# Optimization experiments

Hardware: AMD Instinct MI355X
Metric: run time of the kernel (lower is better)

The kernel has to match this reference:

```python
import jax, jax.numpy as jnp
import numpy as np

N, D, C, P = 256, 1024, 4, 46  # nodes, embedding_dim, max children, num dependency labels
NEG = -1e30  # masked-out candidate value for the max-reduce


def setup_inputs() -> dict:
    key = jax.random.key(0)
    k1, k2 = jax.random.split(key)
    embeddings = jax.random.normal(k1, (N, D), dtype=jnp.float32)
    # Xavier-uniform init of the per-dependency [D,D] matrices, as in _init_params
    scale = float(np.sqrt(6.0 / (D + D)))
    params = jax.random.uniform(k2, (P, D, D), dtype=jnp.float32, minval=-scale, maxval=scale)
    # Build a random tree in topological order: children of node i have index < i;
    # node N-1 is the root. Padded child slots are masked out.
    rng = np.random.default_rng(0)
    c_idx = np.zeros((N, C), dtype=np.int32)
    c_mask = np.zeros((N, C), dtype=bool)
    for i in range(1, N):
        n_children = int(rng.integers(0, C + 1))  # 0 => leaf-like internal node
        c_idx[i] = rng.integers(0, i, size=C)
        c_mask[i, :n_children] = True
    c_mask[N - 1, :] = True  # root always has children
    c_dep = rng.integers(0, P, size=(N, C)).astype(np.int32)
    return {
        "embeddings": embeddings,
        "params": params,
        "children_idx": jnp.asarray(c_idx),
        "children_dep": jnp.asarray(c_dep),
        "children_mask": jnp.asarray(c_mask),
    }


def reference(embeddings, params, children_idx, children_dep, children_mask):
    """Tree-structured dependency encoder.

    For each node i (children first, topological order):
      leaf:     z_i = x_i
      internal: cand_c = params[dep_c] * relu(z_child_c)[None, :]   # [D, D] per child
                mult   = max over children of cand_c                 # [D, D]
                z_i    = x_i @ mult                                  # [D]
    Returns the root embedding, shape [1, D] (matches torch output).
    """
    n_nodes, d = embeddings.shape

    def step(z, inp):
        i, c_idx, c_dep, c_mask = inp
        child_z = jax.nn.relu(z[c_idx])                      # [C, D]
        cand = params[c_dep] * child_z[:, None, :]           # [C, D, D]
        cand = jnp.where(c_mask[:, None, None], cand, NEG)
        mult = jnp.max(cand, axis=0)                         # [D, D]
        x = embeddings[i]                                    # [D]
        z_i = jnp.where(jnp.any(c_mask), x @ mult, x)
        return z.at[i].set(z_i), None

    z0 = jnp.zeros_like(embeddings)
    idxs = jnp.arange(n_nodes)
    z, _ = jax.lax.scan(step, z0, (idxs, children_idx, children_dep, children_mask))
    return z[-1:]  # root node is last in topological order -> [1, D]
```

## Files before the change

kernel.cpp:

```cpp
#include <hip/hip_runtime.h>
#include <hip/hip_fp16.h>
#include <cstddef>

#define NN 256
#define DD 1024
#define CC 4
#define NP 46
#define NT 512
#define ROOT (NN - 1)

__device__ __half g_Pth[NP][DD][DD];

__global__ __launch_bounds__(256) void transpose_kernel(
    const float* __restrict__ par) {
  __shared__ float tile[128][65];
  const int b = blockIdx.x;
  const int p = b >> 7;
  const int t = b & 127;
  const int tr = (t >> 4) << 7;
  const int tc = (t & 15) << 6;
  const int tid = threadIdx.x;
  const float* src = par + ((size_t)p << 20);
  __half* dst = &g_Pth[p][0][0];

#pragma unroll
  for (int k = 0; k < 8; ++k) {
    const int idx = tid + (k << 8);
    const int row = idx >> 4;
    const int c4 = (idx & 15) << 2;
    const float4 v = *(const float4*)(src + (size_t)(tr + row) * DD + tc + c4);
    tile[row][c4 + 0] = v.x;
    tile[row][c4 + 1] = v.y;
    tile[row][c4 + 2] = v.z;
    tile[row][c4 + 3] = v.w;
  }
  __syncthreads();

  const int l = tid & 63;
  const int cb = (tid >> 6) << 4;
  const int r4 = (l & 31) << 2;
#pragma unroll
  for (int m = 0; m < 8; ++m) {
    const int c = cb + (m << 1) + (l >> 5);
    const __half2 h01 = __floats2half2_rn(tile[r4 + 0][c], tile[r4 + 1][c]);
    const __half2 h23 = __floats2half2_rn(tile[r4 + 2][c], tile[r4 + 3][c]);
    const unsigned int u0 = *(const unsigned int*)&h01;
    const unsigned int u1 = *(const unsigned int*)&h23;
    const unsigned long long u =
        (unsigned long long)u0 | ((unsigned long long)u1 << 32);
    __builtin_nontemporal_store(
        u, (unsigned long long*)(dst + (size_t)(tc + c) * DD + tr + r4));
  }
}

struct St {
  float2 p0, p1, p2, p3;
  float x0, x1;
};

__device__ __forceinline__ float4 relu4(float4 v) {
  float4 r;
  r.x = fmaxf(v.x, 0.f); r.y = fmaxf(v.y, 0.f);
  r.z = fmaxf(v.z, 0.f); r.w = fmaxf(v.w, 0.f);
  return r;
}

__device__ __forceinline__ void ld_stage(St& S, int e,
                                         const __half* __restrict__ pt,
                                         const float* __restrict__ emb,
                                         const short* e_meta, const short* e_node,
                                         int j0, int r2) {
  const int meta = e_meta[e];
  const int dep = meta & 0x1FFF;
  const __half* hb = pt + (((size_t)dep) << 20) + (((size_t)j0) << 10) + r2;
  S.p0 = __half22float2(*(const __half2*)(hb));
  S.p1 = __half22float2(*(const __half2*)(hb + DD));
  S.p2 = __half22float2(*(const __half2*)(hb + 2 * DD));
  S.p3 = __half22float2(*(const __half2*)(hb + 3 * DD));
  if (meta & 0x8000) {
    const float2 xx = *(const float2*)(emb + (((size_t)e_node[e]) << 10) + r2);
    S.x0 = xx.x; S.x1 = xx.y;
  }
}

__device__ __forceinline__ float2 mul2s(float2 a, float s) {
  float2 r; r.x = a.x * s; r.y = a.y * s; return r;
}
__device__ __forceinline__ float2 max2(float2 a, float2 b) {
  float2 r; r.x = fmaxf(a.x, b.x); r.y = fmaxf(a.y, b.y); return r;
}

__device__ __forceinline__ void cmp_stage(const St& S, int e, float2& m0, float2& m1,
                                          float2& m2, float2& m3,
                                          float (*z_loc)[4], float (*s_part)[4],
                                          const short* e_child, const short* e_meta,
                                          const short* e_node, int tid) {
  const int meta = e_meta[e];
  const float4 u = relu4(*(const float4*)z_loc[e_child[e]]);
  if (meta & (1 << 14)) {
    m0 = mul2s(S.p0, u.x); m1 = mul2s(S.p1, u.y);
    m2 = mul2s(S.p2, u.z); m3 = mul2s(S.p3, u.w);
  } else {
    m0 = max2(m0, mul2s(S.p0, u.x)); m1 = max2(m1, mul2s(S.p1, u.y));
    m2 = max2(m2, mul2s(S.p2, u.z)); m3 = max2(m3, mul2s(S.p3, u.w));
  }
  if (meta & 0x8000) {
    float4 acc;
    acc.x = fmaf(S.x1, m0.y, S.x0 * m0.x);
    acc.y = fmaf(S.x1, m1.y, S.x0 * m1.x);
    acc.z = fmaf(S.x1, m2.y, S.x0 * m2.x);
    acc.w = fmaf(S.x1, m3.y, S.x0 * m3.x);
#pragma unroll
    for (int off = 1; off < 64; off <<= 1) {
      acc.x += __shfl_xor(acc.x, off, 64);
      acc.y += __shfl_xor(acc.y, off, 64);
      acc.z += __shfl_xor(acc.z, off, 64);
      acc.w += __shfl_xor(acc.w, off, 64);
    }
    if ((tid & 63) == 0) *(float4*)s_part[tid >> 6] = acc;
    __syncthreads();
    if (tid < 4) {
      float s = 0.f;
#pragma unroll
      for (int k = 0; k < 8; ++k) s += s_part[k][tid];
      z_loc[e_node[e]][tid] = s;
    }
    __syncthreads();
  }
}

__global__ __launch_bounds__(NT, 1) void walk_kernel(
    const float* __restrict__ emb, const int* __restrict__ cidx,
    const int* __restrict__ cdep, const unsigned char* __restrict__ cmask,
    float* __restrict__ out) {
  __shared__ float z_loc[NN][4];
  __shared__ short s_ci[NN][CC];
  __shared__ short s_cd[NN][CC];
  __shared__ short s_nc[NN];
  __shared__ int s_pfx[NN];
  __shared__ unsigned char s_reach[NN];
  __shared__ short s_e_child[NN * CC];
  __shared__ short s_e_meta[NN * CC];
  __shared__ short s_e_node[NN * CC];
  __shared__ int s_NE;
  __shared__ int s_flag;
  __shared__ float s_part[8][4];

  const int tid = threadIdx.x;
  const int j0 = blockIdx.x << 2;
  const int r2 = tid << 1;
  const __half* pt = &g_Pth[0][0][0];

  if (tid == 0)
    s_flag = (cmask[1021] == 1 && cmask[1022] == 1 && cmask[1023] == 1);
  __syncthreads();
  const bool m_u8 = (s_flag != 0);
  const int* m32 = (const int*)cmask;
  if (tid < NN) {
    int nc = 0;
#pragma unroll
    for (int c = 0; c < CC; ++c) {
      bool mk = m_u8 ? (cmask[tid * CC + c] != 0) : (m32[tid * CC + c] != 0);
      if (mk) {
        s_ci[tid][nc] = (short)cidx[tid * CC + c];
        s_cd[tid][nc] = (short)cdep[tid * CC + c];
        ++nc;
      }
    }
    s_nc[tid] = (short)nc;
    s_reach[tid] = (tid == ROOT) ? 1 : 0;
  }
  __syncthreads();

  for (int it = 0; it < NN + 2; ++it) {
    if (tid == 0) s_flag = 0;
    __syncthreads();
    if (tid < NN && s_reach[tid] && s_nc[tid] > 0) {
      for (int c = 0; c < s_nc[tid]; ++c) {
        const int ch = s_ci[tid][c];
        if (!s_reach[ch]) { s_reach[ch] = 1; s_flag = 1; }
      }
    }
    __syncthreads();
    const int chg = s_flag;
    __syncthreads();
    if (!chg) break;
  }

  const int wgt = (tid < NN && s_reach[tid] && s_nc[tid] > 0) ? (int)s_nc[tid] : 0;
  if (tid < NN) s_pfx[tid] = wgt;
  __syncthreads();
  for (int off = 1; off < NN; off <<= 1) {
    int v = 0;
    if (tid < NN && tid >= off) v = s_pfx[tid - off];
    __syncthreads();
    if (tid < NN) s_pfx[tid] += v;
    __syncthreads();
  }
  if (tid < NN && wgt > 0) {
    const int st = s_pfx[tid] - wgt;
    for (int c = 0; c < wgt; ++c) {
      s_e_child[st + c] = s_ci[tid][c];
      int meta = (int)s_cd[tid][c];
      if (c == 0) meta |= 1 << 14;
      if (c == wgt - 1) meta |= 1 << 15;
      s_e_meta[st + c] = (short)meta;
      s_e_node[st + c] = (short)tid;
    }
  }
  if (tid == NN - 1) s_NE = s_pfx[NN - 1];

  if (tid < NN) {
    const float4 e = *(const float4*)(emb + (((size_t)tid) << 10) + j0);
    *(float4*)z_loc[tid] = e;
  }
  __syncthreads();
  const int NE = s_NE;

  St A, B, C, D;
  float2 m0, m1, m2, m3;
  if (NE > 0) ld_stage(A, 0, pt, emb, s_e_meta, s_e_node, j0, r2);
  if (NE > 1) ld_stage(B, 1, pt, emb, s_e_meta, s_e_node, j0, r2);
  if (NE > 2) ld_stage(C, 2, pt, emb, s_e_meta, s_e_node, j0, r2);
  int e = 0;
  while (e < NE) {
    if (e + 3 < NE) ld_stage(D, e + 3, pt, emb, s_e_meta, s_e_node, j0, r2);
    cmp_stage(A, e, m0, m1, m2, m3, z_loc, s_part, s_e_child, s_e_meta, s_e_node, tid);
    if (++e >= NE) break;
    if (e + 3 < NE) ld_stage(A, e + 3, pt, emb, s_e_meta, s_e_node, j0, r2);
    cmp_stage(B, e, m0, m1, m2, m3, z_loc, s_part, s_e_child, s_e_meta, s_e_node, tid);
    if (++e >= NE) break;
    if (e + 3 < NE) ld_stage(B, e + 3, pt, emb, s_e_meta, s_e_node, j0, r2);
    cmp_stage(C, e, m0, m1, m2, m3, z_loc, s_part, s_e_child, s_e_meta, s_e_node, tid);
    if (++e >= NE) break;
    if (e + 3 < NE) ld_stage(C, e + 3, pt, emb, s_e_meta, s_e_node, j0, r2);
    cmp_stage(D, e, m0, m1, m2, m3, z_loc, s_part, s_e_child, s_e_meta, s_e_node, tid);
    ++e;
  }

  if (tid < 4) out[j0 + tid] = z_loc[ROOT][tid];
}

extern "C" void kernel_launch(void* const* d_in, const int* in_sizes, int n_in,
                              void* d_out, int out_size, void* d_ws, size_t ws_size,
                              hipStream_t stream) {
  const float* emb = (const float*)d_in[0];
  const float* par = (const float*)d_in[1];
  const int* cidx = (const int*)d_in[2];
  const int* cdep = (const int*)d_in[3];
  const unsigned char* cmask = (const unsigned char*)d_in[4];
  float* out = (float*)d_out;

  hipLaunchKernelGGL(transpose_kernel, dim3(NP * 128), dim3(256), 0, stream, par);
  hipLaunchKernelGGL(walk_kernel, dim3(256), dim3(NT), 0, stream, emb, cidx,
                     cdep, cmask, out);
}
```

Before: 121.7 us.

## Store fp16 transposed params in 64x64 blocked tiles for contiguous per-block reads

The transpose kernel now writes the fp16 parameter copy as 64x64 tiles, each stored contiguously, using 16-byte nontemporal stores. The walk kernel's per-edge loads are re-indexed so each workgroup's four output columns map to a compact 256-element slab per tile. Before, those four columns were spread across four rows 2 KB apart. This aims for better store coalescing in the transpose and better DRAM/cache locality in the walk, at the cost of more transpose blocks and more complex indexing.

```diff
diff --git a/kernel.cpp b/kernel.cpp
--- a/kernel.cpp
+++ b/kernel.cpp
@@ -9,26 +9,28 @@
 #define NT 512
 #define ROOT (NN - 1)
 
-__device__ __half g_Pth[NP][DD][DD];
+typedef unsigned int uint4v __attribute__((ext_vector_type(4)));
+
+__device__ __half g_Pth[NP * DD * DD];
 
 __global__ __launch_bounds__(256) void transpose_kernel(
     const float* __restrict__ par) {
-  __shared__ float tile[128][65];
+  __shared__ float tile[64][65];
   const int b = blockIdx.x;
-  const int p = b >> 7;
-  const int t = b & 127;
-  const int tr = (t >> 4) << 7;
-  const int tc = (t & 15) << 6;
+  const int p = b >> 8;
+  const int t = b & 255;
+  const int jt = t >> 4;
+  const int rt = t & 15;
   const int tid = threadIdx.x;
-  const float* src = par + ((size_t)p << 20);
-  __half* dst = &g_Pth[p][0][0];
-
-#pragma unroll
-  for (int k = 0; k < 8; ++k) {
+  const float* src = par + ((size_t)p << 20) + ((size_t)(rt << 6) << 10) + (jt << 6);
+  __half* dst = g_Pth + (((size_t)(p << 4) + jt) * 16 + rt) * 4096;
+
+#pragma unroll
+  for (int k = 0; k < 4; ++k) {
     const int idx = tid + (k << 8);
     const int row = idx >> 4;
     const int c4 = (idx & 15) << 2;
-    const float4 v = *(const float4*)(src + (size_t)(tr + row) * DD + tc + c4);
+    const float4 v = *(const float4*)(src + (size_t)row * DD + c4);
     tile[row][c4 + 0] = v.x;
     tile[row][c4 + 1] = v.y;
     tile[row][c4 + 2] = v.z;
@@ -36,21 +38,20 @@
   }
   __syncthreads();
 
-  const int l = tid & 63;
-  const int cb = (tid >> 6) << 4;
-  const int r4 = (l & 31) << 2;
-#pragma unroll
-  for (int m = 0; m < 8; ++m) {
-    const int c = cb + (m << 1) + (l >> 5);
-    const __half2 h01 = __floats2half2_rn(tile[r4 + 0][c], tile[r4 + 1][c]);
-    const __half2 h23 = __floats2half2_rn(tile[r4 + 2][c], tile[r4 + 3][c]);
-    const unsigned int u0 = *(const unsigned int*)&h01;
-    const unsigned int u1 = *(const unsigned int*)&h23;
-    const unsigned long long u =
-        (unsigned long long)u0 | ((unsigned long long)u1 << 32);
-    __builtin_nontemporal_store(
-        u, (unsigned long long*)(dst + (size_t)(tc + c) * DD + tr + r4));
-  }
+  const int jq = tid >> 2;
+  const int rq0 = (tid & 3) << 4;
+  unsigned int h[8];
+#pragma unroll
+  for (int i = 0; i < 8; ++i) {
+    const __half2 hh =
+        __floats2half2_rn(tile[rq0 + 2 * i][jq], tile[rq0 + 2 * i + 1][jq]);
+    h[i] = *(const unsigned int*)&hh;
+  }
+  uint4v a = {h[0], h[1], h[2], h[3]};
+  uint4v bq = {h[4], h[5], h[6], h[7]};
+  __half* op = dst + (jq << 6) + rq0;
+  __builtin_nontemporal_store(a, (uint4v*)op);
+  __builtin_nontemporal_store(bq, (uint4v*)(op + 8));
 }
 
 struct St {
@@ -69,14 +70,14 @@
                                          const __half* __restrict__ pt,
                                          const float* __restrict__ emb,
                                          const short* e_meta, const short* e_node,
-                                         int j0, int r2) {
+                                         int jt16, int thr_off, int r2) {
   const int meta = e_meta[e];
   const int dep = meta & 0x1FFF;
-  const __half* hb = pt + (((size_t)dep) << 20) + (((size_t)j0) << 10) + r2;
+  const __half* hb = pt + (((size_t)(dep << 8) + jt16) << 12) + thr_off;
   S.p0 = __half22float2(*(const __half2*)(hb));
-  S.p1 = __half22float2(*(const __half2*)(hb + DD));
-  S.p2 = __half22float2(*(const __half2*)(hb + 2 * DD));
-  S.p3 = __half22float2(*(const __half2*)(hb + 3 * DD));
+  S.p1 = __half22float2(*(const __half2*)(hb + 64));
+  S.p2 = __half22float2(*(const __half2*)(hb + 128));
+  S.p3 = __half22float2(*(const __half2*)(hb + 192));
   if (meta & 0x8000) {
     const float2 xx = *(const float2*)(emb + (((size_t)e_node[e]) << 10) + r2);
     S.x0 = xx.x; S.x1 = xx.y;
@@ -149,7 +150,9 @@
   const int tid = threadIdx.x;
   const int j0 = blockIdx.x << 2;
   const int r2 = tid << 1;
-  const __half* pt = &g_Pth[0][0][0];
+  const __half* pt = g_Pth;
+  const int jt16 = (j0 >> 6) << 4;
+  const int thr_off = ((r2 >> 6) << 12) + ((j0 & 63) << 6) + (r2 & 63);
 
   if (tid == 0)
     s_flag = (cmask[1021] == 1 && cmask[1022] == 1 && cmask[1023] == 1);
@@ -219,21 +222,21 @@
 
   St A, B, C, D;
   float2 m0, m1, m2, m3;
-  if (NE > 0) ld_stage(A, 0, pt, emb, s_e_meta, s_e_node, j0, r2);
-  if (NE > 1) ld_stage(B, 1, pt, emb, s_e_meta, s_e_node, j0, r2);
-  if (NE > 2) ld_stage(C, 2, pt, emb, s_e_meta, s_e_node, j0, r2);
+  if (NE > 0) ld_stage(A, 0, pt, emb, s_e_meta, s_e_node, jt16, thr_off, r2);
+  if (NE > 1) ld_stage(B, 1, pt, emb, s_e_meta, s_e_node, jt16, thr_off, r2);
+  if (NE > 2) ld_stage(C, 2, pt, emb, s_e_meta, s_e_node, jt16, thr_off, r2);
   int e = 0;
   while (e < NE) {
-    if (e + 3 < NE) ld_stage(D, e + 3, pt, emb, s_e_meta, s_e_node, j0, r2);
+    if (e + 3 < NE) ld_stage(D, e + 3, pt, emb, s_e_meta, s_e_node, jt16, thr_off, r2);
     cmp_stage(A, e, m0, m1, m2, m3, z_loc, s_part, s_e_child, s_e_meta, s_e_node, tid);
     if (++e >= NE) break;
-    if (e + 3 < NE) ld_stage(A, e + 3, pt, emb, s_e_meta, s_e_node, j0, r2);
+    if (e + 3 < NE) ld_stage(A, e + 3, pt, emb, s_e_meta, s_e_node, jt16, thr_off, r2);
     cmp_stage(B, e, m0, m1, m2, m3, z_loc, s_part, s_e_child, s_e_meta, s_e_node, tid);
     if (++e >= NE) break;
-    if (e + 3 < NE) ld_stage(B, e + 3, pt, emb, s_e_meta, s_e_node, j0, r2);
+    if (e + 3 < NE) ld_stage(B, e + 3, pt, emb, s_e_meta, s_e_node, jt16, thr_off, r2);
     cmp_stage(C, e, m0, m1, m2, m3, z_loc, s_part, s_e_child, s_e_meta, s_e_node, tid);
     if (++e >= NE) break;
-    if (e + 3 < NE) ld_stage(C, e + 3, pt, emb, s_e_meta, s_e_node, j0, r2);
+    if (e + 3 < NE) ld_stage(C, e + 3, pt, emb, s_e_meta, s_e_node, jt16, thr_off, r2);
     cmp_stage(D, e, m0, m1, m2, m3, z_loc, s_part, s_e_child, s_e_meta, s_e_node, tid);
     ++e;
   }
@@ -251,7 +254,7 @@
   const unsigned char* cmask = (const unsigned char*)d_in[4];
   float* out = (float*)d_out;
 
-  hipLaunchKernelGGL(transpose_kernel, dim3(NP * 128), dim3(256), 0, stream, par);
+  hipLaunchKernelGGL(transpose_kernel, dim3(NP * 256), dim3(256), 0, stream, par);
   hipLaunchKernelGGL(walk_kernel, dim3(256), dim3(NT), 0, stream, emb, cidx,
                      cdep, cmask, out);
 }
```

New measurement: 125.4 us. 3.0% more time.
